# Kernel tuning notes

Measured on AMD Instinct MI355X. Metric: run time of the kernel, lower is better.

## Reference

```python
import jax, jax.numpy as jnp
import numpy as np

EPS = 1e-8
BN_EPS = 1e-5


def _gelu(x):
    return jax.nn.gelu(x, approximate=False)


def _batchnorm(x, gamma, beta):
    # PyTorch BatchNorm1d training-mode: biased variance over the batch dim
    mean = jnp.mean(x, axis=0)
    var = jnp.mean((x - mean) ** 2, axis=0)
    return (x - mean) * jax.lax.rsqrt(var + BN_EPS) * gamma + beta


def setup_inputs() -> dict:
    key = jax.random.key(0)
    N, E, K = 100000, 1600000, 4
    H = 64  # hidden_dim; edge MLP 8 -> H -> H//2 -> H//4
    ks = jax.random.split(key, 16)
    inp = {
        "coords": jax.random.normal(ks[0], (N, 3), jnp.float32),
        "normals": jax.random.normal(ks[1], (N, 3), jnp.float32),
        "curvatures": jax.random.normal(ks[2], (N, K), jnp.float32),
        "edge_index": jax.random.randint(ks[3], (2, E), 0, N, jnp.int64),
        "W1": jax.random.normal(ks[4], (8, H), jnp.float32) * (1.0 / np.sqrt(8)),
        "b1": jnp.zeros((H,), jnp.float32),
        "W2": jax.random.normal(ks[5], (H, H // 2), jnp.float32) * (1.0 / np.sqrt(H)),
        "b2": jnp.zeros((H // 2,), jnp.float32),
        "W3": jax.random.normal(ks[6], (H // 2, H // 4), jnp.float32) * (1.0 / np.sqrt(H // 2)),
        "b3": jnp.zeros((H // 4,), jnp.float32),
        "bn_e_gamma": jnp.ones((H // 4,), jnp.float32),
        "bn_e_beta": jnp.zeros((H // 4,), jnp.float32),
        "Wp": jax.random.normal(ks[7], (H // 4, H // 4), jnp.float32) * (1.0 / np.sqrt(H // 4)),
        "bp": jnp.zeros((H // 4,), jnp.float32),
        "bn_n_gamma": jnp.ones((H // 4,), jnp.float32),
        "bn_n_beta": jnp.zeros((H // 4,), jnp.float32),
    }
    return inp


def reference(coords, normals, curvatures, edge_index,
              W1, b1, W2, b2, W3, b3, bn_e_gamma, bn_e_beta,
              Wp, bp, bn_n_gamma, bn_n_beta):
    N = coords.shape[0]
    D = W3.shape[1]  # hidden_dim // 4
    row, col = edge_index[0], edge_index[1]

    # gather endpoint features per edge
    delta = coords[col] - coords[row]                                   # [E,3]
    n_row, n_col = normals[row], normals[col]
    normal_dot = jnp.sum(n_row * n_col, axis=-1, keepdims=True)         # [E,1]
    dnorm = jnp.linalg.norm(delta, axis=-1, keepdims=True) + EPS
    cos_r = jnp.clip(jnp.sum(n_row * delta, axis=-1, keepdims=True) / dnorm, -1 + EPS, 1 - EPS)
    cos_c = jnp.clip(jnp.sum(n_col * delta, axis=-1, keepdims=True) / dnorm, -1 + EPS, 1 - EPS)
    curv_diff = curvatures[col, :2] - curvatures[row, :2]               # [E,2]
    ef_raw = jnp.concatenate([delta, normal_dot, cos_r, cos_c, curv_diff], axis=-1)  # [E,8]

    # small edge MLP
    h = _gelu(ef_raw @ W1 + b1)
    h = _gelu(h @ W2 + b2)
    ef = h @ W3 + b3                                                    # [E,D]
    ef = _batchnorm(ef, bn_e_gamma, bn_e_beta)

    # scatter edge features to both endpoints with degree normalization
    node_feat = jnp.zeros((N, D), ef.dtype).at[row].add(ef).at[col].add(ef)
    ones = jnp.ones(row.shape, ef.dtype)
    degree = jnp.zeros((N,), ef.dtype).at[row].add(ones).at[col].add(ones)
    degree = jnp.maximum(degree, 1.0)
    node_feat = node_feat / degree[:, None]

    node_feat = node_feat @ Wp + bp
    node_feat = _batchnorm(node_feat, bn_n_gamma, bn_n_beta)
    return node_feat
```

## Files before the change

### kernel.cpp

```cpp
#include <hip/hip_runtime.h>
#include <hip/hip_fp16.h>
#include <math.h>

#define WG 256

typedef _Float16 f16x8 __attribute__((ext_vector_type(8)));
typedef float    f32x4 __attribute__((ext_vector_type(4)));


__device__ __forceinline__ __half2 gelu2(float xa, float xb) {
    float ua = 2.3020885f * xa * fmaf(0.044715f * xa, xa, 1.0f);
    float ub = 2.3020885f * xb * fmaf(0.044715f * xb, xb, 1.0f);
    ua = fminf(fmaxf(ua, -12.12f), 12.12f);
    ub = fminf(fmaxf(ub, -12.12f), 12.12f);
    const __half2 one = __float2half2_rn(1.0f);
    const __half2 xh  = __float22half2_rn(make_float2(xa, xb));
    const __half2 e   = h2exp2(__float22half2_rn(make_float2(ua, ub)));
    const __half2 t   = __hfma2(__float2half2_rn(-2.0f), h2rcp(__hadd2(e, one)), one);
    return __hmul2(__hmul2(__float2half2_rn(0.5f), xh), __hadd2(one, t));
}

#define WAVE_LDS_FENCE() asm volatile("s_waitcnt lgkmcnt(0)" ::: "memory")

__device__ __forceinline__ void acc_h4(f32x4& s, uint2 r) {
    const __half2 ha = *(const __half2*)&r.x;
    const __half2 hb = *(const __half2*)&r.y;
    const float2 fa = __half22float2(ha);
    const float2 fb = __half22float2(hb);
    s[0] += fa.x; s[1] += fa.y; s[2] += fb.x; s[3] += fb.y;
}

__global__ __launch_bounds__(256) void pack_kernel(
    const float* __restrict__ coords, const float* __restrict__ normals,
    const float* __restrict__ curv,
    const float* __restrict__ W1, const float* __restrict__ W2,
    const float* __restrict__ W3,
    float* __restrict__ packed, _Float16* __restrict__ wpk,
    float* __restrict__ stats, int* __restrict__ cnt, int N, int cstr)
{
    const int tid = threadIdx.x;
    for (int n = blockIdx.x * 256 + tid; n < N; n += gridDim.x * 256) {
        const f32x4 lo = {coords[3*n], coords[3*n+1], coords[3*n+2], normals[3*n]};
        const f32x4 hi = {normals[3*n+1], normals[3*n+2], curv[4*n], curv[4*n+1]};
        f32x4* P = (f32x4*)packed;
        P[(size_t)n*2]     = lo;
        P[(size_t)n*2 + 1] = hi;
        cnt[(size_t)n * cstr] = 0;
    }
    if (blockIdx.x == 0) {
        for (int k = tid; k < 512; k += 256) stats[k] = 0.f;
        for (int k = tid; k < 2048; k += 256) {
            const int j = k & 7, col = (k >> 3) & 15, n = (k >> 7) & 3, q = k >> 9;
            wpk[k] = (q == 0) ? (_Float16)W1[j*64 + n*16 + col] : (_Float16)0.f;
        }
        for (int k = tid; k < 2048; k += 256) {
            const int j = k & 7, col = (k >> 3) & 15, q = (k >> 7) & 3,
                      n = (k >> 9) & 1, s = k >> 10;
            wpk[2048 + k] = (_Float16)W2[(s*32 + q*8 + j)*32 + n*16 + col];
        }
        for (int k = tid; k < 512; k += 256) {
            const int j = k & 7, col = (k >> 3) & 15, q = k >> 7;
            wpk[4096 + k] = (_Float16)W3[(q*8 + j)*16 + col];
        }
    }
}

__global__ __launch_bounds__(WG, 4) void edge_mlp_mfma(
    const float* __restrict__ coords,
    const float* __restrict__ normals,
    const float* __restrict__ curv,
    const int*   __restrict__ eidx,
    const float* __restrict__ W1, const float* __restrict__ b1,
    const float* __restrict__ W2, const float* __restrict__ b2,
    const float* __restrict__ W3, const float* __restrict__ b3,
    __half* __restrict__ ef16, int* __restrict__ cnt,
    int* __restrict__ slots, _Float16* __restrict__ ellA,
    int es, int mode, int cstr,
    float* __restrict__ stats, int E,
    const float* __restrict__ packed, const _Float16* __restrict__ wpk)
{
    __shared__ __half h1s[4][32][68];
    __shared__ __half h2s[4][32][36];

    const int t    = threadIdx.x;
    const int w    = t >> 6;
    const int lane = t & 63;
    const int quad = lane >> 4;
    const int col  = lane & 15;

    const int e  = blockIdx.x * WG + w * 64 + lane;
    const bool ev = (e < E);
    const int ec = ev ? e : 0;
    const int r = eidx[ec];
    const int c = eidx[E + ec];

    int pr = 0, qc = 0;
    if (ev) {
        pr = atomicAdd(&cnt[(size_t)r * cstr], 1);
        qc = atomicAdd(&cnt[(size_t)c * cstr], 1);
    }
    const int packR = (ev && pr < es) ? r * es + pr : -1;
    const int packC = (ev && qc < es) ? c * es + qc : -1;

    f16x8 bw1[4];
    f16x8 bw2[2][2];
    f16x8 bw3;
    if (wpk) {
#pragma unroll
        for (int n = 0; n < 4; ++n)
            bw1[n] = *(const f16x8*)(wpk + (((quad*4 + n)*16 + col) << 3));
#pragma unroll
        for (int s = 0; s < 2; ++s)
#pragma unroll
            for (int n = 0; n < 2; ++n)
                bw2[s][n] = *(const f16x8*)(wpk + 2048 +
                                ((((s*2 + n)*4 + quad)*16 + col) << 3));
        bw3 = *(const f16x8*)(wpk + 4096 + ((quad*16 + col) << 3));
    } else {
#pragma unroll
        for (int n = 0; n < 4; ++n) {
#pragma unroll
            for (int j = 0; j < 8; ++j) {
                const int k = quad * 8 + j;
                bw1[n][j] = (k < 8) ? (_Float16)W1[k * 64 + n * 16 + col] : (_Float16)0.f;
            }
        }
#pragma unroll
        for (int s = 0; s < 2; ++s)
#pragma unroll
            for (int n = 0; n < 2; ++n)
#pragma unroll
                for (int j = 0; j < 8; ++j)
                    bw2[s][n][j] = (_Float16)W2[(s * 32 + quad * 8 + j) * 32 + n * 16 + col];
#pragma unroll
        for (int j = 0; j < 8; ++j)
            bw3[j] = (_Float16)W3[(quad * 8 + j) * 16 + col];
    }

    float b1v[4], b2v[2], b3v;
#pragma unroll
    for (int n = 0; n < 4; ++n) b1v[n] = b1[n * 16 + col];
    b2v[0] = b2[col]; b2v[1] = b2[16 + col];
    b3v = b3[col];

    float dx, dy, dz, ndot, cr, cc2, cd0, cd1;
    {
        float rx, ry, rz, nrx, nry, nrz, k0r, k1r;
        float cx, cy, cz, ncx, ncy, ncz, k0c, k1c;
        if (packed) {
            const f32x4* P = (const f32x4*)packed;
            const f32x4 pr0 = P[(size_t)r * 2], pr1 = P[(size_t)r * 2 + 1];
            const f32x4 pc0 = P[(size_t)c * 2], pc1 = P[(size_t)c * 2 + 1];
            rx = pr0[0]; ry = pr0[1]; rz = pr0[2]; nrx = pr0[3];
            nry = pr1[0]; nrz = pr1[1]; k0r = pr1[2]; k1r = pr1[3];
            cx = pc0[0]; cy = pc0[1]; cz = pc0[2]; ncx = pc0[3];
            ncy = pc1[0]; ncz = pc1[1]; k0c = pc1[2]; k1c = pc1[3];
        } else {
            rx = coords[3*r]; ry = coords[3*r+1]; rz = coords[3*r+2];
            cx = coords[3*c]; cy = coords[3*c+1]; cz = coords[3*c+2];
            nrx = normals[3*r]; nry = normals[3*r+1]; nrz = normals[3*r+2];
            ncx = normals[3*c]; ncy = normals[3*c+1]; ncz = normals[3*c+2];
            k0r = curv[4*r]; k1r = curv[4*r+1];
            k0c = curv[4*c]; k1c = curv[4*c+1];
        }
        dx = cx - rx; dy = cy - ry; dz = cz - rz;
        ndot = nrx*ncx + nry*ncy + nrz*ncz;
        const float dn   = sqrtf(dx*dx + dy*dy + dz*dz) + 1e-8f;
        const float inv  = 1.0f / dn;
        const float lo = -1.0f + 1e-8f, hi = 1.0f - 1e-8f;
        cr  = fminf(fmaxf((nrx*dx + nry*dy + nrz*dz) * inv, lo), hi);
        cc2 = fminf(fmaxf((ncx*dx + ncy*dy + ncz*dz) * inv, lo), hi);
        cd0 = k0c - k0r;
        cd1 = k1c - k1r;
    }

    float f[8] = {dx, dy, dz, ndot, cr, cc2, cd0, cd1};
    uint fp[4];
#pragma unroll
    for (int jj = 0; jj < 4; ++jj) {
        const __half2 hh = __float22half2_rn(make_float2(f[2*jj], f[2*jj+1]));
        fp[jj] = *(const uint*)&hh;
    }

    if (mode == 1 && ev) {
        if (pr < es) slots[(size_t)r * es + pr] = e;
        if (qc < es) slots[(size_t)c * es + qc] = e;
    }

    const int e0w = blockIdx.x * WG + w * 64;
    float vsum = 0.f, vsq = 0.f;

#pragma unroll
    for (int p = 0; p < 2; ++p) {
#pragma unroll
        for (int mtl = 0; mtl < 2; ++mtl) {
            const int mt = 2 * p + mtl;
            union { uint u[4]; f16x8 v; } U;
#pragma unroll
            for (int jj = 0; jj < 4; ++jj) {
                const int sv = __shfl((int)fp[jj], (mt << 4) + col, 64);
                U.u[jj] = (quad == 0) ? (uint)sv : 0u;
            }
            const f16x8 a1 = U.v;
            f32x4 c1[4];
#pragma unroll
            for (int n = 0; n < 4; ++n) {
                f32x4 c0 = {b1v[n], b1v[n], b1v[n], b1v[n]};
                c1[n] = __builtin_amdgcn_mfma_f32_16x16x32_f16(a1, bw1[n], c0, 0, 0, 0);
            }
#pragma unroll
            for (int np = 0; np < 2; ++np)
#pragma unroll
                for (int rg = 0; rg < 4; ++rg) {
                    const __half2 g = gelu2(c1[2*np][rg], c1[2*np+1][rg]);
                    __half* dst = &h1s[w][mtl*16 + quad*4 + rg][np*32 + col];
                    dst[0]  = __low2half(g);
                    dst[16] = __high2half(g);
                }
        }
        WAVE_LDS_FENCE();

        f32x4 c2s[2][2];
#pragma unroll
        for (int mtl = 0; mtl < 2; ++mtl) {
            const f16x8 a2s0 = *(const f16x8*)&h1s[w][mtl*16 + col][quad * 8];
            const f16x8 a2s1 = *(const f16x8*)&h1s[w][mtl*16 + col][32 + quad * 8];
#pragma unroll
            for (int n = 0; n < 2; ++n) {
                f32x4 c0 = {b2v[n], b2v[n], b2v[n], b2v[n]};
                c0 = __builtin_amdgcn_mfma_f32_16x16x32_f16(a2s0, bw2[0][n], c0, 0, 0, 0);
                c2s[mtl][n] = __builtin_amdgcn_mfma_f32_16x16x32_f16(a2s1, bw2[1][n], c0, 0, 0, 0);
            }
        }
#pragma unroll
        for (int mtl = 0; mtl < 2; ++mtl)
#pragma unroll
            for (int rg = 0; rg < 4; ++rg) {
                const __half2 g = gelu2(c2s[mtl][0][rg], c2s[mtl][1][rg]);
                __half* dst = &h2s[w][mtl*16 + quad*4 + rg][col];
                dst[0]  = __low2half(g);
                dst[16] = __high2half(g);
            }
        WAVE_LDS_FENCE();

#pragma unroll
        for (int mtl = 0; mtl < 2; ++mtl) {
            const int mt = 2 * p + mtl;
            const f16x8 a3 = *(const f16x8*)&h2s[w][mtl*16 + col][quad * 8];
            f32x4 c0 = {b3v, b3v, b3v, b3v};
            const f32x4 c3 = __builtin_amdgcn_mfma_f32_16x16x32_f16(a3, bw3, c0, 0, 0, 0);

#pragma unroll
            for (int rg = 0; rg < 4; ++rg) {
                const int me = e0w + mt * 16 + quad * 4 + rg;
                if (me < E) { vsum += c3[rg]; vsq += c3[rg] * c3[rg]; }
            }

            if (mode == 2) {
#pragma unroll
                for (int rg = 0; rg < 4; ++rg)
                    h1s[w][mtl*16 + quad*4 + rg][col] = __float2half(c3[rg]);
            } else {
#pragma unroll
                for (int rg = 0; rg < 4; ++rg) {
                    const int me = e0w + mt * 16 + quad * 4 + rg;
                    if (me < E) ef16[(size_t)me * 16 + col] = __float2half(c3[rg]);
                }
            }
        }

        if (mode == 2) {
            WAVE_LDS_FENCE();
            const int j    = lane >> 2;
            const int subl = lane & 3;
#pragma unroll
            for (int mtl = 0; mtl < 2; ++mtl) {
                const int mt = 2 * p + mtl;
                const unsigned long long v =
                    *(const unsigned long long*)&h1s[w][mtl*16 + j][subl * 4];
                const int srcl = (mt << 4) + j;
                const int dR = __shfl(packR, srcl, 64);
                const int dC = __shfl(packC, srcl, 64);
                if (dR >= 0) __builtin_nontemporal_store(v,
                        (unsigned long long*)((char*)ellA + (size_t)dR * 32 + subl * 8));
                if (dC >= 0) __builtin_nontemporal_store(v,
                        (unsigned long long*)((char*)ellA + (size_t)dC * 32 + subl * 8));
            }
        }
    }

    vsum += __shfl_xor(vsum, 16, 64);
    vsq  += __shfl_xor(vsq,  16, 64);
    vsum += __shfl_xor(vsum, 32, 64);
    vsq  += __shfl_xor(vsq,  32, 64);
    float* rp = (float*)&h2s[w][0][0];
    if (lane < 16) {
        rp[col]      = vsum;
        rp[16 + col] = vsq;
    }
    __syncthreads();
    if (t < 32) {
        const float* h2f = (const float*)&h2s[0][0][0];
        const float s = h2f[t] + h2f[576 + t] + h2f[1152 + t] + h2f[1728 + t];
        atomicAdd(&stats[((blockIdx.x & 7) << 5) + t], s);
    }
}

__global__ __launch_bounds__(WG) void gather_seq_kernel(
    const _Float16* __restrict__ ellA, const int* __restrict__ cnt,
    const float* __restrict__ Wp, const float* __restrict__ bp,
    const float* __restrict__ gE, const float* __restrict__ bE,
    float* __restrict__ stats, float* __restrict__ X,
    int N, float invE, int es, int cstr)
{
    __shared__ float sWp[256];
    __shared__ f32x4 syv[4][16][4];
    __shared__ float red2[4][32];

    const int t = threadIdx.x;
    sWp[t] = Wp[t];

    const int w    = t >> 6;
    const int lane = t & 63;
    const int g    = lane >> 2;
    const int subl = lane & 3;
    const int c0   = subl * 4;

    float a[4], bb[4], bpv[4];
#pragma unroll
    for (int cc = 0; cc < 4; ++cc) {
        const int ch = c0 + cc;
        float se = 0.f, sq = 0.f;
#pragma unroll
        for (int rep = 0; rep < 8; ++rep) {
            se += stats[(rep << 5) + ch];
            sq += stats[(rep << 5) + 16 + ch];
        }
        const float mean = se * invE;
        const float var  = sq * invE - mean * mean;
        a[cc]  = gE[ch] * rsqrtf(var + 1e-5f);
        bb[cc] = bE[ch] - mean * a[cc];
        bpv[cc] = bp[ch];
    }

    const int node = blockIdx.x * 64 + w * 16 + g;

    f32x4 s0 = {0.f, 0.f, 0.f, 0.f}, s1 = s0, s2 = s0, s3 = s0;
    int len = 0;
    if (node < N) {
        len = cnt[(size_t)node * cstr];
        const int cap = len < es ? len : es;
        const char* base = (const char*)ellA + (size_t)node * es * 32 + subl * 8;
        int i = 0;
        for (; i + 4 <= cap; i += 4) {
            const uint2 r0 = *(const uint2*)(base + (size_t)(i    ) * 32);
            const uint2 r1 = *(const uint2*)(base + (size_t)(i + 1) * 32);
            const uint2 r2 = *(const uint2*)(base + (size_t)(i + 2) * 32);
            const uint2 r3 = *(const uint2*)(base + (size_t)(i + 3) * 32);
            acc_h4(s0, r0); acc_h4(s1, r1); acc_h4(s2, r2); acc_h4(s3, r3);
        }
        for (; i < cap; ++i) {
            const uint2 r0 = *(const uint2*)(base + (size_t)i * 32);
            acc_h4(s0, r0);
        }
    }

    f32x4 s;
#pragma unroll
    for (int cc = 0; cc < 4; ++cc)
        s[cc] = (s0[cc] + s1[cc]) + (s2[cc] + s3[cc]);

    const float d    = (float)len;
    const float invd = 1.0f / fmaxf(d, 1.0f);
    f32x4 y;
#pragma unroll
    for (int cc = 0; cc < 4; ++cc)
        y[cc] = (a[cc] * s[cc] + bb[cc] * d) * invd;

    syv[w][g][subl] = y;
    __syncthreads();

    const f32x4 y0 = syv[w][g][0];
    const f32x4 y1 = syv[w][g][1];
    const f32x4 y2 = syv[w][g][2];
    const f32x4 y3 = syv[w][g][3];

    const f32x4* sWp4 = (const f32x4*)sWp;
    f32x4 x = {bpv[0], bpv[1], bpv[2], bpv[3]};
#pragma unroll
    for (int j = 0; j < 4; ++j) {
        const f32x4 wj = sWp4[j * 4 + subl];
#pragma unroll
        for (int cc = 0; cc < 4; ++cc) x[cc] += y0[j] * wj[cc];
    }
#pragma unroll
    for (int j = 0; j < 4; ++j) {
        const f32x4 wj = sWp4[(4 + j) * 4 + subl];
#pragma unroll
        for (int cc = 0; cc < 4; ++cc) x[cc] += y1[j] * wj[cc];
    }
#pragma unroll
    for (int j = 0; j < 4; ++j) {
        const f32x4 wj = sWp4[(8 + j) * 4 + subl];
#pragma unroll
        for (int cc = 0; cc < 4; ++cc) x[cc] += y2[j] * wj[cc];
    }
#pragma unroll
    for (int j = 0; j < 4; ++j) {
        const f32x4 wj = sWp4[(12 + j) * 4 + subl];
#pragma unroll
        for (int cc = 0; cc < 4; ++cc) x[cc] += y3[j] * wj[cc];
    }

    if (node < N) {
        *(f32x4*)&X[(size_t)node * 16 + c0] = x;
    } else {
        x = (f32x4){0.f, 0.f, 0.f, 0.f};
    }

    f32x4 vs = x, vq;
#pragma unroll
    for (int cc = 0; cc < 4; ++cc) vq[cc] = x[cc] * x[cc];
#pragma unroll
    for (int off = 4; off <= 32; off <<= 1) {
#pragma unroll
        for (int cc = 0; cc < 4; ++cc) {
            vs[cc] += __shfl_xor(vs[cc], off, 64);
            vq[cc] += __shfl_xor(vq[cc], off, 64);
        }
    }
    if (lane < 4) {
#pragma unroll
        for (int cc = 0; cc < 4; ++cc) {
            red2[w][c0 + cc]      = vs[cc];
            red2[w][16 + c0 + cc] = vq[cc];
        }
    }
    __syncthreads();
    if (t < 32) {
        const float ssum = red2[0][t] + red2[1][t] + red2[2][t] + red2[3][t];
        atomicAdd(&stats[256 + ((blockIdx.x & 7) << 5) + t], ssum);
    }
}

__global__ __launch_bounds__(WG) void scan_blocks_kernel(
    const int* __restrict__ cnt, int* __restrict__ rowptr,
    int* __restrict__ bsum, int N)
{
    __shared__ int sd[WG];
    const int t = threadIdx.x;
    const int i = blockIdx.x * WG + t;
    const int v = (i < N) ? cnt[i] : 0;
    sd[t] = v;
    __syncthreads();
    for (int off = 1; off < WG; off <<= 1) {
        int x = 0;
        if (t >= off) x = sd[t - off];
        __syncthreads();
        sd[t] += x;
        __syncthreads();
    }
    if (i < N) rowptr[i] = sd[t] - v;
    if (t == WG - 1) bsum[blockIdx.x] = sd[t];
}

__global__ __launch_bounds__(512) void scan_top_kernel(
    const int* __restrict__ bsum, int* __restrict__ boff, int nblk)
{
    __shared__ int sd[512];
    const int t = threadIdx.x;
    const int v = (t < nblk) ? bsum[t] : 0;
    sd[t] = v;
    __syncthreads();
    for (int off = 1; off < 512; off <<= 1) {
        int x = 0;
        if (t >= off) x = sd[t - off];
        __syncthreads();
        sd[t] += x;
        __syncthreads();
    }
    if (t < nblk) boff[t] = sd[t] - v;
}

__global__ __launch_bounds__(WG) void scan_add_kernel(
    int* __restrict__ rowptr, int* __restrict__ cursor,
    const int* __restrict__ boff, int N)
{
    const int i = blockIdx.x * WG + threadIdx.x;
    if (i < N) {
        const int v = rowptr[i] + boff[blockIdx.x];
        rowptr[i] = v;
        cursor[i] = v;
    }
}

__global__ __launch_bounds__(WG) void build_kernel(
    const int* __restrict__ eidx, int* __restrict__ cursor,
    int* __restrict__ slots, int E)
{
    const int e = blockIdx.x * WG + threadIdx.x;
    if (e < E) {
        const int r = eidx[e];
        const int c = eidx[E + e];
        const int p = atomicAdd(&cursor[r], 1);
        slots[p] = e;
        const int q = atomicAdd(&cursor[c], 1);
        slots[q] = e;
    }
}

__global__ __launch_bounds__(WG) void gather_kernel(
    const __half* __restrict__ ef16, const int* __restrict__ slots,
    const int* __restrict__ rowptr, const int* __restrict__ cnt,
    const float* __restrict__ Wp, const float* __restrict__ bp,
    const float* __restrict__ gE, const float* __restrict__ bE,
    float* __restrict__ stats, float* __restrict__ X,
    int N, float invE, int es)
{
    __shared__ float sWp[256];
    __shared__ f32x4 syv[4][16][4];
    __shared__ float red2[4][32];

    const int t = threadIdx.x;
    sWp[t] = Wp[t];

    const int w    = t >> 6;
    const int lane = t & 63;
    const int g    = lane >> 2;
    const int subl = lane & 3;
    const int c0   = subl * 4;

    float a[4], bb[4], bpv[4];
#pragma unroll
    for (int cc = 0; cc < 4; ++cc) {
        const int ch = c0 + cc;
        float se = 0.f, sq = 0.f;
#pragma unroll
        for (int rep = 0; rep < 8; ++rep) {
            se += stats[(rep << 5) + ch];
            sq += stats[(rep << 5) + 16 + ch];
        }
        const float mean = se * invE;
        const float var  = sq * invE - mean * mean;
        a[cc]  = gE[ch] * rsqrtf(var + 1e-5f);
        bb[cc] = bE[ch] - mean * a[cc];
        bpv[cc] = bp[ch];
    }

    const int node = blockIdx.x * 64 + w * 16 + g;

    f32x4 s = {0.f, 0.f, 0.f, 0.f};
    int len = 0;
    if (node < N) {
        len = cnt[node];
        const size_t base = (es > 0) ? (size_t)node * (size_t)es : (size_t)rowptr[node];
        const int cap = (es > 0) ? (len < es ? len : es) : len;
        const int* sl = slots + base;
        int i = 0;
        for (; i + 4 <= cap; i += 4) {
            const int e0 = sl[i], e1 = sl[i+1], e2 = sl[i+2], e3 = sl[i+3];
            const uint2 r0 = *(const uint2*)(ef16 + (size_t)e0 * 16 + c0);
            const uint2 r1 = *(const uint2*)(ef16 + (size_t)e1 * 16 + c0);
            const uint2 r2 = *(const uint2*)(ef16 + (size_t)e2 * 16 + c0);
            const uint2 r3 = *(const uint2*)(ef16 + (size_t)e3 * 16 + c0);
            acc_h4(s, r0); acc_h4(s, r1); acc_h4(s, r2); acc_h4(s, r3);
        }
        for (; i < cap; ++i) {
            const uint2 r0 = *(const uint2*)(ef16 + (size_t)sl[i] * 16 + c0);
            acc_h4(s, r0);
        }
    }

    const float d    = (float)len;
    const float invd = 1.0f / fmaxf(d, 1.0f);
    f32x4 y;
#pragma unroll
    for (int cc = 0; cc < 4; ++cc)
        y[cc] = (a[cc] * s[cc] + bb[cc] * d) * invd;

    syv[w][g][subl] = y;
    __syncthreads();

    const f32x4 y0 = syv[w][g][0];
    const f32x4 y1 = syv[w][g][1];
    const f32x4 y2 = syv[w][g][2];
    const f32x4 y3 = syv[w][g][3];

    const f32x4* sWp4 = (const f32x4*)sWp;
    f32x4 x = {bpv[0], bpv[1], bpv[2], bpv[3]};
#pragma unroll
    for (int j = 0; j < 4; ++j) {
        const f32x4 wj = sWp4[j * 4 + subl];
#pragma unroll
        for (int cc = 0; cc < 4; ++cc) x[cc] += y0[j] * wj[cc];
    }
#pragma unroll
    for (int j = 0; j < 4; ++j) {
        const f32x4 wj = sWp4[(4 + j) * 4 + subl];
#pragma unroll
        for (int cc = 0; cc < 4; ++cc) x[cc] += y1[j] * wj[cc];
    }
#pragma unroll
    for (int j = 0; j < 4; ++j) {
        const f32x4 wj = sWp4[(8 + j) * 4 + subl];
#pragma unroll
        for (int cc = 0; cc < 4; ++cc) x[cc] += y2[j] * wj[cc];
    }
#pragma unroll
    for (int j = 0; j < 4; ++j) {
        const f32x4 wj = sWp4[(12 + j) * 4 + subl];
#pragma unroll
        for (int cc = 0; cc < 4; ++cc) x[cc] += y3[j] * wj[cc];
    }

    if (node < N) {
        *(f32x4*)&X[(size_t)node * 16 + c0] = x;
    } else {
        x = (f32x4){0.f, 0.f, 0.f, 0.f};
    }

    f32x4 vs = x, vq;
#pragma unroll
    for (int cc = 0; cc < 4; ++cc) vq[cc] = x[cc] * x[cc];
#pragma unroll
    for (int off = 4; off <= 32; off <<= 1) {
#pragma unroll
        for (int cc = 0; cc < 4; ++cc) {
            vs[cc] += __shfl_xor(vs[cc], off, 64);
            vq[cc] += __shfl_xor(vq[cc], off, 64);
        }
    }
    if (lane < 4) {
#pragma unroll
        for (int cc = 0; cc < 4; ++cc) {
            red2[w][c0 + cc]      = vs[cc];
            red2[w][16 + c0 + cc] = vq[cc];
        }
    }
    __syncthreads();
    if (t < 32) {
        const float ssum = red2[0][t] + red2[1][t] + red2[2][t] + red2[3][t];
        atomicAdd(&stats[256 + ((blockIdx.x & 7) << 5) + t], ssum);
    }
}

__global__ __launch_bounds__(WG) void out_kernel(
    const float* __restrict__ X, const float* __restrict__ stats,
    const float* __restrict__ gN, const float* __restrict__ bN,
    float* __restrict__ out, int total, float invN)
{
    __shared__ float sA[16], sB[16];
    if (threadIdx.x < 16) {
        const int k = threadIdx.x;
        float se = 0.f, sq = 0.f;
#pragma unroll
        for (int rep = 0; rep < 8; ++rep) {
            se += stats[256 + (rep << 5) + k];
            sq += stats[256 + (rep << 5) + 16 + k];
        }
        const float mean = se * invN;
        const float var  = sq * invN - mean * mean;
        const float a    = gN[k] / sqrtf(var + 1e-5f);
        sA[k] = a;
        sB[k] = bN[k] - mean * a;
    }
    __syncthreads();
    const int i = blockIdx.x * WG + threadIdx.x;
    if (i < total) {
        out[i] = sA[i & 15] * X[i] + sB[i & 15];
    }
}


extern "C" void kernel_launch(void* const* d_in, const int* in_sizes, int n_in,
                              void* d_out, int out_size, void* d_ws, size_t ws_size,
                              hipStream_t stream)
{
    const float* coords  = (const float*)d_in[0];
    const float* normals = (const float*)d_in[1];
    const float* curv    = (const float*)d_in[2];
    const int*   eidx    = (const int*)d_in[3];
    const float* W1 = (const float*)d_in[4];
    const float* b1 = (const float*)d_in[5];
    const float* W2 = (const float*)d_in[6];
    const float* b2 = (const float*)d_in[7];
    const float* W3 = (const float*)d_in[8];
    const float* b3 = (const float*)d_in[9];
    const float* gE = (const float*)d_in[10];
    const float* bE = (const float*)d_in[11];
    const float* Wp = (const float*)d_in[12];
    const float* bp = (const float*)d_in[13];
    const float* gN = (const float*)d_in[14];
    const float* bN = (const float*)d_in[15];

    const int N = in_sizes[0] / 3;
    const int E = in_sizes[3] / 2;
    const int eblk = (E + WG - 1) / WG;
    const int nblk = (N + WG - 1) / WG;
    float* out = (float*)d_out;

    const size_t off_cnt  = 4096;
    const size_t ef_bytes = (size_t)E * 32;

    {
        const int es   = 64;
        const int cstr = 16;
        const size_t cnt_bytes = (((size_t)N * cstr * 4) + 255) & ~(size_t)255;
        const size_t ell_bytes = (size_t)N * (size_t)es * 32;
        const size_t need_so   = off_cnt + cnt_bytes + ell_bytes;
        if (ws_size >= need_so) {
            float*    stats = (float*)d_ws;
            int*      cnt   = (int*)((char*)d_ws + off_cnt);
            _Float16* ellA  = (_Float16*)((char*)d_ws + off_cnt + cnt_bytes);

            const size_t off_pk = need_so;
            const size_t off_wp = off_pk + (size_t)N * 32;
            const bool   ext    = (ws_size >= off_wp + 9216);
            float*    packed = ext ? (float*)((char*)d_ws + off_pk) : nullptr;
            _Float16* wpk    = ext ? (_Float16*)((char*)d_ws + off_wp) : nullptr;

            if (ext) {
                pack_kernel<<<dim3((N + 255) / 256), dim3(256), 0, stream>>>(
                    coords, normals, curv, W1, W2, W3, packed, wpk, stats, cnt, N, cstr);
            } else {
                hipMemsetAsync(d_ws, 0, off_cnt + cnt_bytes, stream);
            }

            edge_mlp_mfma<<<dim3(eblk), dim3(WG), 0, stream>>>(
                coords, normals, curv, eidx, W1, b1, W2, b2, W3, b3,
                (__half*)nullptr, cnt, (int*)nullptr, ellA, es, 2, cstr, stats, E,
                packed, wpk);

            gather_seq_kernel<<<dim3((N + 63) / 64), dim3(WG), 0, stream>>>(
                ellA, cnt, Wp, bp, gE, bE, stats, out, N, 1.0f / (float)E, es, cstr);

            out_kernel<<<dim3((N * 16 + WG - 1) / WG), dim3(WG), 0, stream>>>(
                out, stats, gN, bN, out, N * 16, 1.0f / (float)N);
            return;
        }
    }

    {
        const size_t cnt_bytes = (((size_t)N * 4) + 255) & ~(size_t)255;
        const size_t off_slots = off_cnt + cnt_bytes;
        int es = 0;
        const int strides[3] = {96, 80, 64};
        for (int si = 0; si < 3; ++si) {
            const size_t need = off_slots + (size_t)N * (size_t)strides[si] * 4 + ef_bytes;
            if (need <= ws_size) { es = strides[si]; break; }
        }
        if (es > 0) {
            float*  stats = (float*)d_ws;
            int*    cnt   = (int*)((char*)d_ws + off_cnt);
            int*    slots = (int*)((char*)d_ws + off_slots);
            __half* ef16  = (__half*)((char*)d_ws + off_slots + (size_t)N * (size_t)es * 4);

            hipMemsetAsync(d_ws, 0, off_cnt + (size_t)N * 4, stream);

            edge_mlp_mfma<<<dim3(eblk), dim3(WG), 0, stream>>>(
                coords, normals, curv, eidx, W1, b1, W2, b2, W3, b3,
                ef16, cnt, slots, (_Float16*)nullptr, es, 1, 1, stats, E,
                nullptr, nullptr);

            gather_kernel<<<dim3((N + 63) / 64), dim3(WG), 0, stream>>>(
                ef16, slots, cnt, cnt, Wp, bp, gE, bE, stats, out,
                N, 1.0f / (float)E, es);

            out_kernel<<<dim3((N * 16 + WG - 1) / WG), dim3(WG), 0, stream>>>(
                out, stats, gN, bN, out, N * 16, 1.0f / (float)N);
            return;
        }
    }

    const size_t need_csr = off_cnt + (size_t)(3 * (size_t)N + 8192 + 2 * (size_t)E) * 4
                          + ef_bytes + 256;
    if (ws_size >= need_csr && nblk <= 4096) {
        float*  stats  = (float*)d_ws;
        int*    cnt    = (int*)((char*)d_ws + off_cnt);
        int*    rowptr = cnt + N;
        int*    cursor = rowptr + N;
        int*    bsum   = cursor + N;
        int*    boff   = bsum + 4096;
        int*    slots  = boff + 4096;
        __half* ef16   = (__half*)(slots + 2 * (size_t)E);

        hipMemsetAsync(d_ws, 0, off_cnt + (size_t)N * 4, stream);

        edge_mlp_mfma<<<dim3(eblk), dim3(WG), 0, stream>>>(
            coords, normals, curv, eidx, W1, b1, W2, b2, W3, b3,
            ef16, cnt, slots, (_Float16*)nullptr, 0, 0, 1, stats, E,
            nullptr, nullptr);

        scan_blocks_kernel<<<dim3(nblk), dim3(WG), 0, stream>>>(cnt, rowptr, bsum, N);
        scan_top_kernel<<<dim3(1), dim3(512), 0, stream>>>(bsum, boff, nblk);
        scan_add_kernel<<<dim3(nblk), dim3(WG), 0, stream>>>(rowptr, cursor, boff, N);
        build_kernel<<<dim3((E + WG - 1) / WG), dim3(WG), 0, stream>>>(eidx, cursor, slots, E);

        gather_kernel<<<dim3((N + 63) / 64), dim3(WG), 0, stream>>>(
            ef16, slots, rowptr, cnt, Wp, bp, gE, bE, stats, out,
            N, 1.0f / (float)E, 0);

        out_kernel<<<dim3((N * 16 + WG - 1) / WG), dim3(WG), 0, stream>>>(
            out, stats, gN, bN, out, N * 16, 1.0f / (float)N);
        return;
    }
}
```

Measured before the change: 300.7 us.

## Widen ELL slot stores and gathers to 16-byte accesses with 8 lanes per node

The edge MLP now writes each edge's 16 fp16 features to the ELL slot array as two 16-byte nontemporal stores per edge (one per lane pair) instead of four 8-byte stores. The gather kernel assigns 8 lanes per node, each loading a 16-byte half-row from interleaved slots, and reduces across lanes with shuffles. The projection output is split into 2 channels per lane, and the grid now covers 32 nodes per block. The aim is fewer, wider memory transactions in both the scatter and the gather, with more lanes per node to hide latency. The cost is extra shuffle reductions, and the per-node loop becomes less balanced for short neighbour lists.

```diff
diff --git a/kernel.cpp b/kernel.cpp
--- a/kernel.cpp
+++ b/kernel.cpp
@@ -6,6 +6,7 @@
 
 typedef _Float16 f16x8 __attribute__((ext_vector_type(8)));
 typedef float    f32x4 __attribute__((ext_vector_type(4)));
+typedef unsigned int u32x4 __attribute__((ext_vector_type(4)));
 
 
 __device__ __forceinline__ __half2 gelu2(float xa, float xb) {
@@ -257,9 +258,10 @@
             }
 
             if (mode == 2) {
+                __half* stage = &h1s[w][0][0];
 #pragma unroll
                 for (int rg = 0; rg < 4; ++rg)
-                    h1s[w][mtl*16 + quad*4 + rg][col] = __float2half(c3[rg]);
+                    stage[(mtl*16 + quad*4 + rg) * 16 + col] = __float2half(c3[rg]);
             } else {
 #pragma unroll
                 for (int rg = 0; rg < 4; ++rg) {
@@ -271,21 +273,17 @@
 
         if (mode == 2) {
             WAVE_LDS_FENCE();
-            const int j    = lane >> 2;
-            const int subl = lane & 3;
-#pragma unroll
-            for (int mtl = 0; mtl < 2; ++mtl) {
-                const int mt = 2 * p + mtl;
-                const unsigned long long v =
-                    *(const unsigned long long*)&h1s[w][mtl*16 + j][subl * 4];
-                const int srcl = (mt << 4) + j;
-                const int dR = __shfl(packR, srcl, 64);
-                const int dC = __shfl(packC, srcl, 64);
-                if (dR >= 0) __builtin_nontemporal_store(v,
-                        (unsigned long long*)((char*)ellA + (size_t)dR * 32 + subl * 8));
-                if (dC >= 0) __builtin_nontemporal_store(v,
-                        (unsigned long long*)((char*)ellA + (size_t)dC * 32 + subl * 8));
-            }
+            const __half* stage = &h1s[w][0][0];
+            const int row32 = lane >> 1;
+            const int half  = lane & 1;
+            const u32x4 v = *(const u32x4*)(stage + row32 * 16 + half * 8);
+            const int srcl = ((2 * p + (row32 >> 4)) << 4) + (row32 & 15);
+            const int dR = __shfl(packR, srcl, 64);
+            const int dC = __shfl(packC, srcl, 64);
+            if (dR >= 0) __builtin_nontemporal_store(v,
+                    (u32x4*)((char*)ellA + (size_t)dR * 32 + half * 16));
+            if (dC >= 0) __builtin_nontemporal_store(v,
+                    (u32x4*)((char*)ellA + (size_t)dC * 32 + half * 16));
         }
     }
 
@@ -314,127 +312,137 @@
     int N, float invE, int es, int cstr)
 {
     __shared__ float sWp[256];
-    __shared__ f32x4 syv[4][16][4];
+    __shared__ float syv[4][8][20];
     __shared__ float red2[4][32];
 
     const int t = threadIdx.x;
     sWp[t] = Wp[t];
+    __syncthreads();
 
     const int w    = t >> 6;
     const int lane = t & 63;
-    const int g    = lane >> 2;
-    const int subl = lane & 3;
-    const int c0   = subl * 4;
-
-    float a[4], bb[4], bpv[4];
+    const int g8   = lane >> 3;
+    const int s8   = lane & 7;
+    const int half = s8 & 1;
+    const int rowo = s8 >> 1;
+    const int hb   = half * 8;
+
+    f32x4 seA = {0.f,0.f,0.f,0.f}, seB = seA, sqA = seA, sqB = seA;
+#pragma unroll
+    for (int rep = 0; rep < 8; ++rep) {
+        const float* sp = stats + (rep << 5);
+        seA += *(const f32x4*)(sp + hb);
+        seB += *(const f32x4*)(sp + hb + 4);
+        sqA += *(const f32x4*)(sp + 16 + hb);
+        sqB += *(const f32x4*)(sp + 16 + hb + 4);
+    }
+    const f32x4 gEA = *(const f32x4*)(gE + hb), gEB = *(const f32x4*)(gE + hb + 4);
+    const f32x4 bEA = *(const f32x4*)(bE + hb), bEB = *(const f32x4*)(bE + hb + 4);
+    f32x4 aA, aB, bbA, bbB;
 #pragma unroll
     for (int cc = 0; cc < 4; ++cc) {
-        const int ch = c0 + cc;
-        float se = 0.f, sq = 0.f;
-#pragma unroll
-        for (int rep = 0; rep < 8; ++rep) {
-            se += stats[(rep << 5) + ch];
-            sq += stats[(rep << 5) + 16 + ch];
-        }
-        const float mean = se * invE;
-        const float var  = sq * invE - mean * mean;
-        a[cc]  = gE[ch] * rsqrtf(var + 1e-5f);
-        bb[cc] = bE[ch] - mean * a[cc];
-        bpv[cc] = bp[ch];
-    }
-
-    const int node = blockIdx.x * 64 + w * 16 + g;
-
-    f32x4 s0 = {0.f, 0.f, 0.f, 0.f}, s1 = s0, s2 = s0, s3 = s0;
+        float mean = seA[cc] * invE;
+        float var  = sqA[cc] * invE - mean * mean;
+        aA[cc]  = gEA[cc] * rsqrtf(var + 1e-5f);
+        bbA[cc] = bEA[cc] - mean * aA[cc];
+        mean = seB[cc] * invE;
+        var  = sqB[cc] * invE - mean * mean;
+        aB[cc]  = gEB[cc] * rsqrtf(var + 1e-5f);
+        bbB[cc] = bEB[cc] - mean * aB[cc];
+    }
+
+    const int node = blockIdx.x * 32 + w * 8 + g8;
+
+    f32x4 sA = {0.f,0.f,0.f,0.f}, sB = sA;
     int len = 0;
     if (node < N) {
         len = cnt[(size_t)node * cstr];
         const int cap = len < es ? len : es;
-        const char* base = (const char*)ellA + (size_t)node * es * 32 + subl * 8;
-        int i = 0;
-        for (; i + 4 <= cap; i += 4) {
-            const uint2 r0 = *(const uint2*)(base + (size_t)(i    ) * 32);
-            const uint2 r1 = *(const uint2*)(base + (size_t)(i + 1) * 32);
-            const uint2 r2 = *(const uint2*)(base + (size_t)(i + 2) * 32);
-            const uint2 r3 = *(const uint2*)(base + (size_t)(i + 3) * 32);
-            acc_h4(s0, r0); acc_h4(s1, r1); acc_h4(s2, r2); acc_h4(s3, r3);
-        }
-        for (; i < cap; ++i) {
-            const uint2 r0 = *(const uint2*)(base + (size_t)i * 32);
-            acc_h4(s0, r0);
-        }
-    }
-
-    f32x4 s;
-#pragma unroll
-    for (int cc = 0; cc < 4; ++cc)
-        s[cc] = (s0[cc] + s1[cc]) + (s2[cc] + s3[cc]);
+        const char* base = (const char*)ellA + (size_t)node * es * 32
+                         + (size_t)rowo * 32 + (size_t)half * 16;
+        for (int i = 0; 4 * i + rowo < cap; ++i) {
+            const u32x4 v = *(const u32x4*)(base + (size_t)i * 128);
+            const __half2* h = (const __half2*)&v;
+            const float2 f0 = __half22float2(h[0]);
+            const float2 f1 = __half22float2(h[1]);
+            const float2 f2 = __half22float2(h[2]);
+            const float2 f3 = __half22float2(h[3]);
+            sA[0] += f0.x; sA[1] += f0.y; sA[2] += f1.x; sA[3] += f1.y;
+            sB[0] += f2.x; sB[1] += f2.y; sB[2] += f3.x; sB[3] += f3.y;
+        }
+    }
+#pragma unroll
+    for (int off = 2; off <= 4; off <<= 1) {
+#pragma unroll
+        for (int cc = 0; cc < 4; ++cc) {
+            sA[cc] += __shfl_xor(sA[cc], off, 64);
+            sB[cc] += __shfl_xor(sB[cc], off, 64);
+        }
+    }
 
     const float d    = (float)len;
     const float invd = 1.0f / fmaxf(d, 1.0f);
-    f32x4 y;
-#pragma unroll
-    for (int cc = 0; cc < 4; ++cc)
-        y[cc] = (a[cc] * s[cc] + bb[cc] * d) * invd;
-
-    syv[w][g][subl] = y;
-    __syncthreads();
-
-    const f32x4 y0 = syv[w][g][0];
-    const f32x4 y1 = syv[w][g][1];
-    const f32x4 y2 = syv[w][g][2];
-    const f32x4 y3 = syv[w][g][3];
-
-    const f32x4* sWp4 = (const f32x4*)sWp;
-    f32x4 x = {bpv[0], bpv[1], bpv[2], bpv[3]};
-#pragma unroll
-    for (int j = 0; j < 4; ++j) {
-        const f32x4 wj = sWp4[j * 4 + subl];
-#pragma unroll
-        for (int cc = 0; cc < 4; ++cc) x[cc] += y0[j] * wj[cc];
-    }
-#pragma unroll
-    for (int j = 0; j < 4; ++j) {
-        const f32x4 wj = sWp4[(4 + j) * 4 + subl];
-#pragma unroll
-        for (int cc = 0; cc < 4; ++cc) x[cc] += y1[j] * wj[cc];
-    }
-#pragma unroll
-    for (int j = 0; j < 4; ++j) {
-        const f32x4 wj = sWp4[(8 + j) * 4 + subl];
-#pragma unroll
-        for (int cc = 0; cc < 4; ++cc) x[cc] += y2[j] * wj[cc];
-    }
-#pragma unroll
-    for (int j = 0; j < 4; ++j) {
-        const f32x4 wj = sWp4[(12 + j) * 4 + subl];
-#pragma unroll
-        for (int cc = 0; cc < 4; ++cc) x[cc] += y3[j] * wj[cc];
+    f32x4 yA, yB;
+#pragma unroll
+    for (int cc = 0; cc < 4; ++cc) {
+        yA[cc] = (aA[cc] * sA[cc] + bbA[cc] * d) * invd;
+        yB[cc] = (aB[cc] * sB[cc] + bbB[cc] * d) * invd;
+    }
+
+    if (s8 < 2) {
+        *(f32x4*)&syv[w][g8][hb]     = yA;
+        *(f32x4*)&syv[w][g8][hb + 4] = yB;
+    }
+    WAVE_LDS_FENCE();
+
+    const f32x4 y0 = *(const f32x4*)&syv[w][g8][0];
+    const f32x4 y1 = *(const f32x4*)&syv[w][g8][4];
+    const f32x4 y2 = *(const f32x4*)&syv[w][g8][8];
+    const f32x4 y3 = *(const f32x4*)&syv[w][g8][12];
+
+    const int j0 = s8 * 2;
+    const float2* sWp2 = (const float2*)sWp;
+    float2 x2 = {bp[j0], bp[j0 + 1]};
+#pragma unroll
+    for (int k = 0; k < 4; ++k) {
+        const float2 wv = sWp2[k * 8 + s8];
+        x2.x += y0[k] * wv.x; x2.y += y0[k] * wv.y;
+    }
+#pragma unroll
+    for (int k = 0; k < 4; ++k) {
+        const float2 wv = sWp2[(4 + k) * 8 + s8];
+        x2.x += y1[k] * wv.x; x2.y += y1[k] * wv.y;
+    }
+#pragma unroll
+    for (int k = 0; k < 4; ++k) {
+        const float2 wv = sWp2[(8 + k) * 8 + s8];
+        x2.x += y2[k] * wv.x; x2.y += y2[k] * wv.y;
+    }
+#pragma unroll
+    for (int k = 0; k < 4; ++k) {
+        const float2 wv = sWp2[(12 + k) * 8 + s8];
+        x2.x += y3[k] * wv.x; x2.y += y3[k] * wv.y;
     }
 
     if (node < N) {
-        *(f32x4*)&X[(size_t)node * 16 + c0] = x;
+        *(float2*)&X[(size_t)node * 16 + j0] = x2;
     } else {
-        x = (f32x4){0.f, 0.f, 0.f, 0.f};
-    }
-
-    f32x4 vs = x, vq;
-#pragma unroll
-    for (int cc = 0; cc < 4; ++cc) vq[cc] = x[cc] * x[cc];
-#pragma unroll
-    for (int off = 4; off <= 32; off <<= 1) {
-#pragma unroll
-        for (int cc = 0; cc < 4; ++cc) {
-            vs[cc] += __shfl_xor(vs[cc], off, 64);
-            vq[cc] += __shfl_xor(vq[cc], off, 64);
-        }
-    }
-    if (lane < 4) {
-#pragma unroll
-        for (int cc = 0; cc < 4; ++cc) {
-            red2[w][c0 + cc]      = vs[cc];
-            red2[w][16 + c0 + cc] = vq[cc];
-        }
+        x2 = make_float2(0.f, 0.f);
+    }
+
+    float vsx = x2.x, vsy = x2.y, vqx = x2.x * x2.x, vqy = x2.y * x2.y;
+#pragma unroll
+    for (int off = 8; off <= 32; off <<= 1) {
+        vsx += __shfl_xor(vsx, off, 64);
+        vsy += __shfl_xor(vsy, off, 64);
+        vqx += __shfl_xor(vqx, off, 64);
+        vqy += __shfl_xor(vqy, off, 64);
+    }
+    if (lane < 8) {
+        red2[w][j0]          = vsx;
+        red2[w][j0 + 1]      = vsy;
+        red2[w][16 + j0]     = vqx;
+        red2[w][16 + j0 + 1] = vqy;
     }
     __syncthreads();
     if (t < 32) {
@@ -731,7 +739,7 @@
                 (__half*)nullptr, cnt, (int*)nullptr, ellA, es, 2, cstr, stats, E,
                 packed, wpk);
 
-            gather_seq_kernel<<<dim3((N + 63) / 64), dim3(WG), 0, stream>>>(
+            gather_seq_kernel<<<dim3((N + 31) / 32), dim3(WG), 0, stream>>>(
                 ellA, cnt, Wp, bp, gE, bE, stats, out, N, 1.0f / (float)E, es, cstr);
 
             out_kernel<<<dim3((N * 16 + WG - 1) / WG), dim3(WG), 0, stream>>>(
```

New measurement: 336.5 us. 1.12x slower.
